# Optimization experiments

Hardware: AMD Instinct MI355X
Metric: run time of the kernel (lower is better)

## Reference

```python
import jax, jax.numpy as jnp
import numpy as np

NUM_PREFIXES = 64  # == head_dim in this config


def setup_inputs() -> dict:
    key = jax.random.key(0)
    ks = jax.random.split(key, 12)
    B, S, H = 2, 2048, 1024
    hd = NUM_PREFIXES
    nh = H // hd              # 16 heads
    din = dout = 128
    kg = H // dout            # key conv groups = 8
    P = S + hd                # position_dim = 2112
    f = jnp.float32
    sc = 0.02
    hidden = jax.random.normal(ks[0], (B, S, H), f)
    # one-hot positions: prefix tokens (first hd) use slots [S, S+hd), rest use their index
    idx = jnp.where(jnp.arange(S) < hd, S + jnp.arange(S), jnp.arange(S))
    pos = jnp.broadcast_to(jax.nn.one_hot(idx, P, dtype=f)[None], (B, S, P))
    mask = jnp.ones((B, 1, S, S), f)  # peak_into_future=True -> full visibility
    return {
        "hidden_states": hidden,
        "position_embeddings": pos,
        "attention_mask": mask,
        "Wq_head": sc * jax.random.normal(ks[1], (hd, nh, nh), f),
        "Wk_group": sc * jax.random.normal(ks[2], (kg, din, din), f),
        "Wk_head": sc * jax.random.normal(ks[3], (dout, kg, kg), f),
        "Wv_head": sc * jax.random.normal(ks[4], (hd, nh, nh), f),
        "p_attn": sc * jax.random.normal(ks[5], (3 * hd, P), f),
        "p_expand": sc * jax.random.normal(ks[6], (3, 1, nh), f),
        "Wc": sc * jax.random.normal(ks[7], (hd, nh, nh), f),
        "Wg": sc * jax.random.normal(ks[8], (2, H), f),
        "Ug": sc * jax.random.normal(ks[9], (2, H), f),
        "Vg": sc * jax.random.normal(ks[10], (2, P), f),
        "bg": jnp.zeros((2,), f),
    }


def reference(hidden_states, position_embeddings, attention_mask,
              Wq_head, Wk_group, Wk_head, Wv_head,
              p_attn, p_expand, Wc, Wg, Ug, Vg, bg):
    B, S, H = hidden_states.shape
    hd, nh, _ = Wq_head.shape
    kg, din, _ = Wk_group.shape
    npf = NUM_PREFIXES
    # LinearDescent.forward: zero out prefix-prefix attention block
    mask = attention_mask.at[:, :, :npf, :npf].set(0.0)
    # --- Attention: conv2d/per-dim head-mixing projections (proj_conv2d, proj_transpose) ---
    xh = hidden_states.reshape(B, S, nh, hd)
    q = jnp.einsum('bshd,dhg->bsgd', xh, Wq_head)      # per-dim mixing across heads
    v = jnp.einsum('bshd,dhg->bsgd', xh, Wv_head)
    # key path: per-group linear (kg groups of din), then per-dim mixing across groups
    xg = hidden_states.reshape(B, S, kg, din)
    k1 = jnp.einsum('bsgd,gde->bsge', xg, Wk_group)
    k2 = jnp.einsum('bsgd,dgh->bshd', k1, Wk_head)     # (B,S,kg,dout)
    k = k2.reshape(B, S, nh, hd)
    # positional q/k/v via p_attn (3*hd x P) + per-head expansion via p_expand (3,1,nh)
    pqkv = jnp.einsum('bsp,cp->bsc', position_embeddings, p_attn).reshape(B, S, 3, hd)
    q = q + p_expand[0, 0][None, None, :, None] * pqkv[:, :, 0][:, :, None, :]
    k = k + p_expand[1, 0][None, None, :, None] * pqkv[:, :, 1][:, :, None, :]
    v = v + p_expand[2, 0][None, None, :, None] * pqkv[:, :, 2][:, :, None, :]
    # linear (non-softmax) attention with multiplicative mask, no causal mask
    scores = jnp.einsum('bqhd,bkhd->bhqk', q, k) * mask
    ctx = jnp.einsum('bhqk,bkhd->bqhd', scores, v)
    out = jnp.einsum('bqhd,dhg->bqgd', ctx, Wc).reshape(B, S, H)
    # --- Gates: two sigmoid gates from hidden, attention output, and positions ---
    g = jax.nn.sigmoid(hidden_states @ Wg.T + out @ Ug.T + position_embeddings @ Vg.T + bg)
    return g[..., 0:1] * out + g[..., 1:2] * hidden_states
```

## Files before the change

### kernel.cpp

```cpp
#include <hip/hip_runtime.h>
#include <math.h>

#define SS   2048
#define PP   2112
#define C3   192
#define PQS  196
#define NZCAP 16

__device__ __forceinline__ void fma4s(float4& a, float s, const float4& b) {
    a.x += s*b.x; a.y += s*b.y; a.z += s*b.z; a.w += s*b.w;
}
__device__ __forceinline__ void fme4(float4& a, const float4& x, const float4& w) {
    a.x += x.x*w.x; a.y += x.y*w.y; a.z += x.z*w.z; a.w += x.w*w.w;
}
__device__ __forceinline__ float comp(const float4& v, int j) {
    return j==0 ? v.x : j==1 ? v.y : j==2 ? v.z : v.w;
}
__device__ __forceinline__ float dot4(const float4& a, const float4& b) {
    return a.x*b.x + a.y*b.y + a.z*b.z + a.w*b.w;
}

__global__ __launch_bounds__(256) void kp_prep(
    const float* __restrict__ Wq, const float* __restrict__ Wv,
    const float* __restrict__ Wc, const float* __restrict__ Wkh,
    const float* __restrict__ Wkg, const float* __restrict__ p_attn,
    const float* __restrict__ pos, const float* __restrict__ Vg,
    float* __restrict__ WqT, float* __restrict__ WvT, float* __restrict__ WcT,
    float* __restrict__ WkhT, float* __restrict__ WkgT, float* __restrict__ pqg)
{
    const int t = threadIdx.x, blk = blockIdx.x;
    if (blk < 48) {
        const float* src = (blk < 16) ? Wq : (blk < 32) ? Wv : Wc;
        float* dst = (blk < 16) ? WqT : (blk < 32) ? WvT : WcT;
        int base = (blk & 15) * 1024;
        #pragma unroll
        for (int i = 0; i < 4; ++i) {
            int didx = base + i*256 + t;
            int d = didx & 63, g = (didx>>6)&15, h = didx>>10;
            dst[didx] = src[(d<<8)+(h<<4)+g];
        }
        return;
    } else if (blk < 56) {
        int base = (blk-48)*1024;
        #pragma unroll
        for (int i = 0; i < 4; ++i) {
            int didx = base + i*256 + t;
            int dk = didx&127, hk = (didx>>7)&7, g = didx>>10;
            WkhT[didx] = Wkh[dk*64 + g*8 + hk];
        }
        return;
    } else if (blk < 184) {
        int base = (blk-56)*1024;
        #pragma unroll
        for (int i = 0; i < 4; ++i) {
            int didx = base + i*256 + t;
            int e = didx&127, g = (didx>>7)&7, d = didx>>10;
            WkgT[didx] = Wkg[(g*128+d)*128 + e];
        }
        return;
    }

    __shared__ float pq[4][C3+4];
    __shared__ int   cnt[4];
    __shared__ int   plist[4][NZCAP];
    __shared__ float vlist[4][NZCAP];
    const int row0 = (blk - 184) * 4;

    for (int i = t; i < 4*(C3+4); i += 256) ((float*)pq)[i] = 0.f;
    if (t < 4) cnt[t] = 0;
    __syncthreads();

    #pragma unroll
    for (int r = 0; r < 4; ++r) {
        const float4* prow4 = (const float4*)(pos + (size_t)(row0+r)*PP);
        #pragma unroll
        for (int c = 0; c < 3; ++c) {
            int fi = c*256 + t;
            if (fi < PP/4) {
                float4 v4 = prow4[fi];
                float vals[4] = {v4.x, v4.y, v4.z, v4.w};
                #pragma unroll
                for (int u = 0; u < 4; ++u) if (vals[u] != 0.f) {
                    int idx = atomicAdd(&cnt[r], 1);
                    if (idx < NZCAP) { plist[r][idx] = fi*4+u; vlist[r][idx] = vals[u]; }
                    else {
                        int p = fi*4+u; float val = vals[u];
                        for (int cc = 0; cc < C3; ++cc)
                            atomicAdd(&pq[r][cc], val * p_attn[(size_t)cc*PP + p]);
                        atomicAdd(&pq[r][C3],   val * Vg[p]);
                        atomicAdd(&pq[r][C3+1], val * Vg[PP+p]);
                    }
                }
            }
        }
    }
    __syncthreads();

    #pragma unroll
    for (int r = 0; r < 4; ++r) {
        int n = min(cnt[r], NZCAP);
        float acc = (t < C3+2) ? pq[r][t] : 0.f;
        for (int i = 0; i < n; ++i) {
            int p = plist[r][i]; float val = vlist[r][i];
            if (t < C3)           acc += val * p_attn[(size_t)t*PP + p];
            else if (t == C3)     acc += val * Vg[p];
            else if (t == C3+1)   acc += val * Vg[PP+p];
        }
        if (t < C3+2) pqg[(size_t)(row0+r)*PQS + t] = acc;
    }
}

__global__ __launch_bounds__(256, 4) void ka_proj(
    const float* __restrict__ hidden, const float* __restrict__ pqg,
    const float* __restrict__ WkgT, const float* __restrict__ WkhT,
    const float* __restrict__ WvT,  const float* __restrict__ p_exp,
    float* __restrict__ ko, float* __restrict__ vo)
{
    __shared__ __align__(16) float xs[4][1024];
    const int t = threadIdx.x;
    const int row0 = blockIdx.x * 4;

    #pragma unroll
    for (int i = 0; i < 4; ++i)
        ((float4*)xs)[i*256+t] = ((const float4*)hidden)[(size_t)row0*256 + i*256 + t];
    __syncthreads();

    {
        const int g = t>>4, dq = t&15;
        const float4* WvT4 = (const float4*)WvT;
        const float pev = p_exp[32+g];
        float4 av[4];
        #pragma unroll
        for (int r = 0; r < 4; ++r) {
            float4 pv = *(const float4*)(pqg + (size_t)(row0+r)*PQS + 128 + dq*4);
            av[r] = make_float4(pev*pv.x, pev*pv.y, pev*pv.z, pev*pv.w);
        }
        #pragma unroll 4
        for (int h = 0; h < 16; ++h) {
            float4 w = WvT4[(h*16+g)*16+dq];
            #pragma unroll
            for (int r = 0; r < 4; ++r)
                fme4(av[r], ((const float4*)xs[r])[h*16+dq], w);
        }
        #pragma unroll
        for (int r = 0; r < 4; ++r)
            ((float4*)vo)[(size_t)(row0+r)*256 + g*16 + dq] = av[r];
    }

    float4 a1[4] = {};
    {
        const int g8 = t>>5, eq = t&31;
        const float4* WkgT4 = (const float4*)WkgT;
        for (int dq = 0; dq < 32; ++dq) {
            float4 xq[4];
            #pragma unroll
            for (int r = 0; r < 4; ++r) xq[r] = ((const float4*)xs[r])[g8*32 + dq];
            #pragma unroll
            for (int j = 0; j < 4; ++j) {
                int d = dq*4 + j;
                float4 w = WkgT4[(d*8+g8)*32 + eq];
                #pragma unroll
                for (int r = 0; r < 4; ++r) fma4s(a1[r], comp(xq[r], j), w);
            }
        }
    }
    __syncthreads();
    {
        const int g8 = t>>5, eq = t&31;
        #pragma unroll
        for (int r = 0; r < 4; ++r)
            ((float4*)xs[r])[g8*32 + eq] = a1[r];
    }
    __syncthreads();

    {
        const int hk = t>>5, dkq = t&31;
        const int hh = hk*2 + (dkq>>4);
        const float pe = p_exp[16 + hh];
        const float4* WkhT4 = (const float4*)WkhT;
        float4 acc[4];
        #pragma unroll
        for (int r = 0; r < 4; ++r) {
            float4 pk = *(const float4*)(pqg + (size_t)(row0+r)*PQS + 64 + (dkq&15)*4);
            acc[r] = make_float4(pe*pk.x, pe*pk.y, pe*pk.z, pe*pk.w);
        }
        #pragma unroll
        for (int g = 0; g < 8; ++g) {
            float4 w = WkhT4[(g*8+hk)*32 + dkq];
            #pragma unroll
            for (int r = 0; r < 4; ++r)
                fme4(acc[r], ((const float4*)xs[r])[g*32 + dkq], w);
        }
        #pragma unroll
        for (int r = 0; r < 4; ++r)
            ((float4*)ko)[(size_t)(row0+r)*256 + hk*32 + dkq] = acc[r];
    }
}

__global__ __launch_bounds__(256) void km_kv(
    const float* __restrict__ k, const float* __restrict__ v,
    float* __restrict__ Mpart)
{
    __shared__ __align__(16) float kt[2048];
    __shared__ __align__(16) float vt[2048];
    const int t  = threadIdx.x;
    const int c  = blockIdx.x >> 5;
    const int bh = blockIdx.x & 31;
    const int b  = bh >> 4, h = bh & 15;
    const int et = t>>4, dt = t&15;
    float acc[4][4] = {};

    #pragma unroll
    for (int tile = 0; tile < 2; ++tile) {
        const int r0 = c*64 + tile*32;
        #pragma unroll
        for (int i = 0; i < 2; ++i) {
            int fi = t + 256*i;
            int r = fi>>4, q4 = fi&15;
            size_t ga = (size_t)(b*SS + r0 + r)*256 + h*16 + q4;
            ((float4*)kt)[fi] = ((const float4*)k)[ga];
            ((float4*)vt)[fi] = ((const float4*)v)[ga];
        }
        __syncthreads();
        #pragma unroll 4
        for (int r = 0; r < 32; ++r) {
            float4 kk = ((const float4*)kt)[r*16+et];
            float4 vv = ((const float4*)vt)[r*16+dt];
            float ka[4]={kk.x,kk.y,kk.z,kk.w}, va[4]={vv.x,vv.y,vv.z,vv.w};
            #pragma unroll
            for (int i2=0;i2<4;++i2)
                #pragma unroll
                for (int j=0;j<4;++j) acc[i2][j] += ka[i2]*va[j];
        }
        __syncthreads();
    }
    float4* Mc = (float4*)(Mpart + ((size_t)c*32 + bh)*4096);
    #pragma unroll
    for (int i2=0;i2<4;++i2) {
        float4 o = {acc[i2][0],acc[i2][1],acc[i2][2],acc[i2][3]};
        Mc[(et*4+i2)*16 + dt] = o;
    }
}

__global__ __launch_bounds__(256) void kr_red(
    const float* __restrict__ Mpart,
    float* __restrict__ Mfull, float* __restrict__ Mdiff)
{
    int qid = blockIdx.x*256 + threadIdx.x;
    int bh = qid >> 10, inner = qid & 1023;
    float4 s = {0,0,0,0};
    #pragma unroll
    for (int c = 1; c < 32; ++c) {
        float4 m = ((const float4*)Mpart)[(((size_t)c*32 + bh)<<10) + inner];
        s.x+=m.x; s.y+=m.y; s.z+=m.z; s.w+=m.w;
    }
    ((float4*)Mdiff)[qid] = s;
    float4 m0 = ((const float4*)Mpart)[((size_t)bh<<10) + inner];
    s.x+=m0.x; s.y+=m0.y; s.z+=m0.z; s.w+=m0.w;
    ((float4*)Mfull)[qid] = s;
}

__global__ __launch_bounds__(256, 4) void kb_out(
    const float* __restrict__ hidden, const float* __restrict__ pqg,
    const float* __restrict__ Mfull,  const float* __restrict__ Mdiff,
    const float* __restrict__ WqT,    const float* __restrict__ p_exp,
    const float* __restrict__ WcT,    const float* __restrict__ Wg,
    const float* __restrict__ Ug,     const float* __restrict__ bg,
    float* __restrict__ yo)
{
    __shared__ __align__(16) float xs[4][1024];
    __shared__ __align__(16) float qs[4][1024];
    __shared__ __align__(16) float pq0s[4][64];
    __shared__ float gs[16];
    const int t  = threadIdx.x;
    const int b  = blockIdx.x >> 9;
    const int s0 = (blockIdx.x & 511) * 4;
    const size_t rqbase = ((size_t)b*SS + s0) * 256;

    float4 xv[4];
    #pragma unroll
    for (int r = 0; r < 4; ++r) {
        xv[r] = ((const float4*)hidden)[rqbase + r*256 + t];
        ((float4*)xs[r])[t] = xv[r];
    }
    if (t < 64) {
        int r = t>>4, q = t&15;
        ((float4*)pq0s[r])[q] = *(const float4*)(pqg + (size_t)(b*SS + s0 + r)*PQS + q*4);
    }
    if (t < 16) gs[t] = 0.f;
    __syncthreads();

    const int g = t>>4, dq = t&15;

    float pW0[4], pW1[4];
    {
        float4 w0 = ((const float4*)Wg)[t], w1 = ((const float4*)Wg)[256+t];
        #pragma unroll
        for (int r = 0; r < 4; ++r) {
            pW0[r] = dot4(xv[r], w0);
            pW1[r] = dot4(xv[r], w1);
        }
    }

    {
        const float4* WqT4 = (const float4*)WqT;
        const float peq = p_exp[g];
        float4 aq[4];
        #pragma unroll
        for (int r = 0; r < 4; ++r) {
            aq[r] = make_float4(0.f, 0.f, 0.f, 0.f);
            fma4s(aq[r], peq, ((const float4*)pq0s[r])[dq]);
        }
        #pragma unroll 4
        for (int h = 0; h < 16; ++h) {
            float4 w = WqT4[(h*16+g)*16+dq];
            #pragma unroll
            for (int r = 0; r < 4; ++r)
                fme4(aq[r], ((const float4*)xs[r])[h*16+dq], w);
        }
        #pragma unroll
        for (int r = 0; r < 4; ++r) ((float4*)qs[r])[t] = aq[r];
    }
    __syncthreads();

    {
        const float* Msel = (s0 < 64) ? Mdiff : Mfull;
        const float4* Mb = (const float4*)Msel + ((size_t)b*16 + g)*1024;
        float4 acc[4] = {};
        #pragma unroll 2
        for (int eq = 0; eq < 16; ++eq) {
            float4 qq[4];
            #pragma unroll
            for (int r = 0; r < 4; ++r)
                qq[r] = ((const float4*)qs[r])[g*16 + eq];
            #pragma unroll
            for (int j = 0; j < 4; ++j) {
                float4 m = Mb[(eq*4+j)*16 + dq];
                #pragma unroll
                for (int r = 0; r < 4; ++r) fma4s(acc[r], comp(qq[r],j), m);
            }
        }
        #pragma unroll
        for (int r = 0; r < 4; ++r) ((float4*)xs[r])[t] = acc[r];
    }
    __syncthreads();

    float4 oo[4] = {};
    float pU0[4], pU1[4];
    {
        const float4* WcT4 = (const float4*)WcT;
        #pragma unroll 4
        for (int h = 0; h < 16; ++h) {
            float4 w = WcT4[(h*16+g)*16+dq];
            #pragma unroll
            for (int r = 0; r < 4; ++r)
                fme4(oo[r], ((const float4*)xs[r])[h*16+dq], w);
        }
        float4 u0 = ((const float4*)Ug)[t], u1 = ((const float4*)Ug)[256+t];
        #pragma unroll
        for (int r = 0; r < 4; ++r) {
            pU0[r] = dot4(oo[r], u0);
            pU1[r] = dot4(oo[r], u1);
        }
    }

    #pragma unroll
    for (int r = 0; r < 4; ++r) {
        float v0 = pW0[r], v1 = pW1[r], v2 = pU0[r], v3 = pU1[r];
        #pragma unroll
        for (int off = 32; off > 0; off >>= 1) {
            v0 += __shfl_down(v0, off);
            v1 += __shfl_down(v1, off);
            v2 += __shfl_down(v2, off);
            v3 += __shfl_down(v3, off);
        }
        if ((t & 63) == 0) {
            atomicAdd(&gs[r*4+0], v0);
            atomicAdd(&gs[r*4+1], v1);
            atomicAdd(&gs[r*4+2], v2);
            atomicAdd(&gs[r*4+3], v3);
        }
    }
    __syncthreads();

    #pragma unroll
    for (int r = 0; r < 4; ++r) {
        size_t grow = (size_t)b*SS + s0 + r;
        float z0 = gs[r*4+0] + gs[r*4+2] + pqg[grow*PQS + 192] + bg[0];
        float z1 = gs[r*4+1] + gs[r*4+3] + pqg[grow*PQS + 193] + bg[1];
        float G0 = 1.f/(1.f+expf(-z0));
        float G1 = 1.f/(1.f+expf(-z1));
        float4 y;
        y.x = G0*oo[r].x + G1*xv[r].x;
        y.y = G0*oo[r].y + G1*xv[r].y;
        y.z = G0*oo[r].z + G1*xv[r].z;
        y.w = G0*oo[r].w + G1*xv[r].w;
        ((float4*)yo)[rqbase + r*256 + t] = y;
    }
}

extern "C" void kernel_launch(void* const* d_in, const int* in_sizes, int n_in,
                              void* d_out, int out_size, void* d_ws, size_t ws_size,
                              hipStream_t stream)
{
    const float* hidden = (const float*)d_in[0];
    const float* pos    = (const float*)d_in[1];
    const float* Wq     = (const float*)d_in[3];
    const float* Wkg    = (const float*)d_in[4];
    const float* Wkh    = (const float*)d_in[5];
    const float* Wv     = (const float*)d_in[6];
    const float* p_attn = (const float*)d_in[7];
    const float* p_exp  = (const float*)d_in[8];
    const float* Wc     = (const float*)d_in[9];
    const float* Wg     = (const float*)d_in[10];
    const float* Ug     = (const float*)d_in[11];
    const float* Vg     = (const float*)d_in[12];
    const float* bg     = (const float*)d_in[13];

    float* ws    = (float*)d_ws;
    float* ko    = ws;
    float* vo    = ws + 4194304;
    float* Mpart = ws + 8388608;
    float* Mfull = ws + 12582912;
    float* Mdiff = ws + 12713984;
    float* pqg   = ws + 12845056;
    float* WqT   = ws + 13647872;
    float* WvT   = ws + 13664256;
    float* WcT   = ws + 13680640;
    float* WkhT  = ws + 13697024;
    float* WkgT  = ws + 13705216;

    kp_prep<<<dim3(1208), dim3(256), 0, stream>>>(Wq, Wv, Wc, Wkh, Wkg, p_attn,
                                                  pos, Vg, WqT, WvT, WcT, WkhT,
                                                  WkgT, pqg);
    ka_proj<<<dim3(1024), dim3(256), 0, stream>>>(hidden, pqg, WkgT, WkhT, WvT,
                                                  p_exp, ko, vo);
    km_kv<<<dim3(1024), dim3(256), 0, stream>>>(ko, vo, Mpart);
    kr_red<<<dim3(128), dim3(256), 0, stream>>>(Mpart, Mfull, Mdiff);
    kb_out<<<dim3(1024), dim3(256), 0, stream>>>(hidden, pqg, Mfull, Mdiff,
                                                 WqT, p_exp, WcT, Wg, Ug, bg,
                                                 (float*)d_out);
}
```

Baseline: 216.6 us.

## Fuse all five stages into one cooperative persistent kernel with grid syncs

Adds a single cooperative kernel that runs weight transposes, positional projection, K/V projection, KV outer-product partials, reduction and the output/gate stage, separated by grid-wide syncs. It keeps each block's hidden-state rows in shared memory across stages, so they are not reloaded in the final stage, and it removes four kernel launch boundaries. The old multi-kernel path remains as a fallback when cooperative launch is unavailable or fails. The cost is four grid barriers, and 1024 blocks must be co-resident (launch bounds of 4 blocks per CU), which may lower occupancy per stage.

```diff
diff --git a/kernel.cpp b/kernel.cpp
--- a/kernel.cpp
+++ b/kernel.cpp
@@ -1,5 +1,8 @@
 #include <hip/hip_runtime.h>
+#include <hip/hip_cooperative_groups.h>
 #include <math.h>
+
+namespace cg = cooperative_groups;
 
 #define SS   2048
 #define PP   2112
@@ -18,6 +21,361 @@
 }
 __device__ __forceinline__ float dot4(const float4& a, const float4& b) {
     return a.x*b.x + a.y*b.y + a.z*b.z + a.w*b.w;
+}
+
+__global__ __launch_bounds__(256, 4) void mega_ld(
+    const float* __restrict__ hidden, const float* __restrict__ pos,
+    const float* __restrict__ Wq, const float* __restrict__ Wkg,
+    const float* __restrict__ Wkh, const float* __restrict__ Wv,
+    const float* __restrict__ p_attn, const float* __restrict__ p_exp,
+    const float* __restrict__ Wc, const float* __restrict__ Wg,
+    const float* __restrict__ Ug, const float* __restrict__ Vg,
+    const float* __restrict__ bg,
+    float* __restrict__ ko, float* __restrict__ vo,
+    float* __restrict__ Mpart, float* __restrict__ Mfull,
+    float* __restrict__ Mdiff, float* __restrict__ pqg,
+    float* __restrict__ WqT, float* __restrict__ WvT,
+    float* __restrict__ WcT, float* __restrict__ WkhT,
+    float* __restrict__ WkgT, float* __restrict__ yo)
+{
+    cg::grid_group grid = cg::this_grid();
+    __shared__ __align__(16) float smem[8464];
+    float (*xs)[1024] = (float(*)[1024])smem;
+    float* region2    = smem + 4096;
+    float (*pq0s)[64] = (float(*)[64])(smem + 8192);
+    float* gs         = smem + 8448;
+
+    const int t = threadIdx.x, blk = blockIdx.x;
+    const int row0 = blk * 4;
+
+    #pragma unroll
+    for (int i = 0; i < 4; ++i)
+        ((float4*)xs)[i*256+t] = ((const float4*)hidden)[(size_t)row0*256 + i*256 + t];
+
+    if (blk < 48) {
+        const float* src = (blk < 16) ? Wq : (blk < 32) ? Wv : Wc;
+        float* dst = (blk < 16) ? WqT : (blk < 32) ? WvT : WcT;
+        int base = (blk & 15) * 1024;
+        #pragma unroll
+        for (int i = 0; i < 4; ++i) {
+            int didx = base + i*256 + t;
+            int d = didx & 63, g = (didx>>6)&15, h = didx>>10;
+            dst[didx] = src[(d<<8)+(h<<4)+g];
+        }
+    } else if (blk < 56) {
+        int base = (blk-48)*1024;
+        #pragma unroll
+        for (int i = 0; i < 4; ++i) {
+            int didx = base + i*256 + t;
+            int dk = didx&127, hk = (didx>>7)&7, g = didx>>10;
+            WkhT[didx] = Wkh[dk*64 + g*8 + hk];
+        }
+    } else if (blk < 184) {
+        int base = (blk-56)*1024;
+        #pragma unroll
+        for (int i = 0; i < 4; ++i) {
+            int didx = base + i*256 + t;
+            int e = didx&127, g = (didx>>7)&7, d = didx>>10;
+            WkgT[didx] = Wkg[(g*128+d)*128 + e];
+        }
+    }
+
+    {
+        float (*pq)[C3+4]    = (float(*)[C3+4])region2;
+        int*   cnt           = (int*)(region2 + 784);
+        int  (*plist)[NZCAP] = (int(*)[NZCAP])(region2 + 788);
+        float(*vlist)[NZCAP] = (float(*)[NZCAP])(region2 + 788 + 4*NZCAP);
+
+        for (int i = t; i < 4*(C3+4); i += 256) ((float*)pq)[i] = 0.f;
+        if (t < 4) cnt[t] = 0;
+        __syncthreads();
+
+        #pragma unroll
+        for (int r = 0; r < 4; ++r) {
+            const float4* prow4 = (const float4*)(pos + (size_t)(row0+r)*PP);
+            #pragma unroll
+            for (int c = 0; c < 3; ++c) {
+                int fi = c*256 + t;
+                if (fi < PP/4) {
+                    float4 v4 = prow4[fi];
+                    float vals[4] = {v4.x, v4.y, v4.z, v4.w};
+                    #pragma unroll
+                    for (int u = 0; u < 4; ++u) if (vals[u] != 0.f) {
+                        int idx = atomicAdd(&cnt[r], 1);
+                        if (idx < NZCAP) { plist[r][idx] = fi*4+u; vlist[r][idx] = vals[u]; }
+                        else {
+                            int p = fi*4+u; float val = vals[u];
+                            for (int cc = 0; cc < C3; ++cc)
+                                atomicAdd(&pq[r][cc], val * p_attn[(size_t)cc*PP + p]);
+                            atomicAdd(&pq[r][C3],   val * Vg[p]);
+                            atomicAdd(&pq[r][C3+1], val * Vg[PP+p]);
+                        }
+                    }
+                }
+            }
+        }
+        __syncthreads();
+
+        #pragma unroll
+        for (int r = 0; r < 4; ++r) {
+            int n = min(cnt[r], NZCAP);
+            float acc = (t < C3+2) ? pq[r][t] : 0.f;
+            for (int i = 0; i < n; ++i) {
+                int p = plist[r][i]; float val = vlist[r][i];
+                if (t < C3)           acc += val * p_attn[(size_t)t*PP + p];
+                else if (t == C3)     acc += val * Vg[p];
+                else if (t == C3+1)   acc += val * Vg[PP+p];
+            }
+            if (t < C3+2) pqg[(size_t)(row0+r)*PQS + t] = acc;
+        }
+    }
+    grid.sync();
+
+    {
+        const int g = t>>4, dq = t&15;
+        const float4* WvT4 = (const float4*)WvT;
+        const float pev = p_exp[32+g];
+        float4 av[4];
+        #pragma unroll
+        for (int r = 0; r < 4; ++r) {
+            float4 pv = *(const float4*)(pqg + (size_t)(row0+r)*PQS + 128 + dq*4);
+            av[r] = make_float4(pev*pv.x, pev*pv.y, pev*pv.z, pev*pv.w);
+        }
+        #pragma unroll 4
+        for (int h = 0; h < 16; ++h) {
+            float4 w = WvT4[(h*16+g)*16+dq];
+            #pragma unroll
+            for (int r = 0; r < 4; ++r)
+                fme4(av[r], ((const float4*)xs[r])[h*16+dq], w);
+        }
+        #pragma unroll
+        for (int r = 0; r < 4; ++r)
+            ((float4*)vo)[(size_t)(row0+r)*256 + g*16 + dq] = av[r];
+    }
+    {
+        float (*k1s)[1024] = (float(*)[1024])region2;
+        float4 a1[4] = {};
+        const int g8 = t>>5, eq = t&31;
+        const float4* WkgT4 = (const float4*)WkgT;
+        for (int dq = 0; dq < 32; ++dq) {
+            float4 xq[4];
+            #pragma unroll
+            for (int r = 0; r < 4; ++r) xq[r] = ((const float4*)xs[r])[g8*32 + dq];
+            #pragma unroll
+            for (int j = 0; j < 4; ++j) {
+                int d = dq*4 + j;
+                float4 w = WkgT4[(d*8+g8)*32 + eq];
+                #pragma unroll
+                for (int r = 0; r < 4; ++r) fma4s(a1[r], comp(xq[r], j), w);
+            }
+        }
+        #pragma unroll
+        for (int r = 0; r < 4; ++r)
+            ((float4*)k1s[r])[g8*32 + eq] = a1[r];
+        __syncthreads();
+
+        const int hk = t>>5, dkq = t&31;
+        const int hh = hk*2 + (dkq>>4);
+        const float pe = p_exp[16 + hh];
+        const float4* WkhT4 = (const float4*)WkhT;
+        float4 acc[4];
+        #pragma unroll
+        for (int r = 0; r < 4; ++r) {
+            float4 pk = *(const float4*)(pqg + (size_t)(row0+r)*PQS + 64 + (dkq&15)*4);
+            acc[r] = make_float4(pe*pk.x, pe*pk.y, pe*pk.z, pe*pk.w);
+        }
+        #pragma unroll
+        for (int g = 0; g < 8; ++g) {
+            float4 w = WkhT4[(g*8+hk)*32 + dkq];
+            #pragma unroll
+            for (int r = 0; r < 4; ++r)
+                fme4(acc[r], ((const float4*)k1s[r])[g*32 + dkq], w);
+        }
+        #pragma unroll
+        for (int r = 0; r < 4; ++r)
+            ((float4*)ko)[(size_t)(row0+r)*256 + hk*32 + dkq] = acc[r];
+    }
+    grid.sync();
+
+    {
+        float* kt = region2;
+        float* vt = region2 + 2048;
+        const int c = blk>>5, bh = blk&31, b = bh>>4, h = bh&15;
+        const int et = t>>4, dt = t&15;
+        float acc[4][4] = {};
+        #pragma unroll
+        for (int tile = 0; tile < 2; ++tile) {
+            const int r0 = c*64 + tile*32;
+            #pragma unroll
+            for (int i = 0; i < 2; ++i) {
+                int fi = t + 256*i;
+                int r = fi>>4, q4 = fi&15;
+                size_t ga = (size_t)(b*SS + r0 + r)*256 + h*16 + q4;
+                ((float4*)kt)[fi] = ((const float4*)ko)[ga];
+                ((float4*)vt)[fi] = ((const float4*)vo)[ga];
+            }
+            __syncthreads();
+            #pragma unroll 4
+            for (int r = 0; r < 32; ++r) {
+                float4 kk = ((const float4*)kt)[r*16+et];
+                float4 vv = ((const float4*)vt)[r*16+dt];
+                float ka[4]={kk.x,kk.y,kk.z,kk.w}, va[4]={vv.x,vv.y,vv.z,vv.w};
+                #pragma unroll
+                for (int i2=0;i2<4;++i2)
+                    #pragma unroll
+                    for (int j=0;j<4;++j) acc[i2][j] += ka[i2]*va[j];
+            }
+            __syncthreads();
+        }
+        float4* Mc = (float4*)(Mpart + ((size_t)c*32 + bh)*4096);
+        #pragma unroll
+        for (int i2=0;i2<4;++i2) {
+            float4 o = {acc[i2][0],acc[i2][1],acc[i2][2],acc[i2][3]};
+            Mc[(et*4+i2)*16 + dt] = o;
+        }
+    }
+    grid.sync();
+
+    if (blk < 128) {
+        int qid = blk*256 + t;
+        int bh = qid >> 10, inner = qid & 1023;
+        float4 s = {0,0,0,0};
+        #pragma unroll
+        for (int c = 1; c < 32; ++c) {
+            float4 m = ((const float4*)Mpart)[(((size_t)c*32 + bh)<<10) + inner];
+            s.x+=m.x; s.y+=m.y; s.z+=m.z; s.w+=m.w;
+        }
+        ((float4*)Mdiff)[qid] = s;
+        float4 m0 = ((const float4*)Mpart)[((size_t)bh<<10) + inner];
+        s.x+=m0.x; s.y+=m0.y; s.z+=m0.z; s.w+=m0.w;
+        ((float4*)Mfull)[qid] = s;
+    }
+    grid.sync();
+
+    {
+        float (*qs)[1024] = (float(*)[1024])region2;
+        const int b  = blk >> 9;
+        const int s0 = (blk & 511) * 4;
+        const size_t rqbase = ((size_t)b*SS + s0) * 256;
+
+        float4 xv[4];
+        #pragma unroll
+        for (int r = 0; r < 4; ++r) xv[r] = ((const float4*)xs[r])[t];
+        if (t < 64) {
+            int r = t>>4, q = t&15;
+            ((float4*)pq0s[r])[q] = *(const float4*)(pqg + (size_t)(b*SS + s0 + r)*PQS + q*4);
+        }
+        if (t < 16) gs[t] = 0.f;
+        __syncthreads();
+
+        const int g = t>>4, dq = t&15;
+
+        float pW0[4], pW1[4];
+        {
+            float4 w0 = ((const float4*)Wg)[t], w1 = ((const float4*)Wg)[256+t];
+            #pragma unroll
+            for (int r = 0; r < 4; ++r) {
+                pW0[r] = dot4(xv[r], w0);
+                pW1[r] = dot4(xv[r], w1);
+            }
+        }
+
+        {
+            const float4* WqT4 = (const float4*)WqT;
+            const float peq = p_exp[g];
+            float4 aq[4];
+            #pragma unroll
+            for (int r = 0; r < 4; ++r) {
+                aq[r] = make_float4(0.f, 0.f, 0.f, 0.f);
+                fma4s(aq[r], peq, ((const float4*)pq0s[r])[dq]);
+            }
+            #pragma unroll 4
+            for (int h = 0; h < 16; ++h) {
+                float4 w = WqT4[(h*16+g)*16+dq];
+                #pragma unroll
+                for (int r = 0; r < 4; ++r)
+                    fme4(aq[r], ((const float4*)xs[r])[h*16+dq], w);
+            }
+            #pragma unroll
+            for (int r = 0; r < 4; ++r) ((float4*)qs[r])[t] = aq[r];
+        }
+        __syncthreads();
+
+        {
+            const float* Msel = (s0 < 64) ? Mdiff : Mfull;
+            const float4* Mb = (const float4*)Msel + ((size_t)b*16 + g)*1024;
+            float4 acc[4] = {};
+            #pragma unroll 2
+            for (int eq = 0; eq < 16; ++eq) {
+                float4 qq[4];
+                #pragma unroll
+                for (int r = 0; r < 4; ++r)
+                    qq[r] = ((const float4*)qs[r])[g*16 + eq];
+                #pragma unroll
+                for (int j = 0; j < 4; ++j) {
+                    float4 m = Mb[(eq*4+j)*16 + dq];
+                    #pragma unroll
+                    for (int r = 0; r < 4; ++r) fma4s(acc[r], comp(qq[r],j), m);
+                }
+            }
+            #pragma unroll
+            for (int r = 0; r < 4; ++r) ((float4*)xs[r])[t] = acc[r];
+        }
+        __syncthreads();
+
+        float4 oo[4] = {};
+        float pU0[4], pU1[4];
+        {
+            const float4* WcT4 = (const float4*)WcT;
+            #pragma unroll 4
+            for (int h = 0; h < 16; ++h) {
+                float4 w = WcT4[(h*16+g)*16+dq];
+                #pragma unroll
+                for (int r = 0; r < 4; ++r)
+                    fme4(oo[r], ((const float4*)xs[r])[h*16+dq], w);
+            }
+            float4 u0 = ((const float4*)Ug)[t], u1 = ((const float4*)Ug)[256+t];
+            #pragma unroll
+            for (int r = 0; r < 4; ++r) {
+                pU0[r] = dot4(oo[r], u0);
+                pU1[r] = dot4(oo[r], u1);
+            }
+        }
+
+        #pragma unroll
+        for (int r = 0; r < 4; ++r) {
+            float v0 = pW0[r], v1 = pW1[r], v2 = pU0[r], v3 = pU1[r];
+            #pragma unroll
+            for (int off = 32; off > 0; off >>= 1) {
+                v0 += __shfl_down(v0, off);
+                v1 += __shfl_down(v1, off);
+                v2 += __shfl_down(v2, off);
+                v3 += __shfl_down(v3, off);
+            }
+            if ((t & 63) == 0) {
+                atomicAdd(&gs[r*4+0], v0);
+                atomicAdd(&gs[r*4+1], v1);
+                atomicAdd(&gs[r*4+2], v2);
+                atomicAdd(&gs[r*4+3], v3);
+            }
+        }
+        __syncthreads();
+
+        #pragma unroll
+        for (int r = 0; r < 4; ++r) {
+            size_t grow = (size_t)b*SS + s0 + r;
+            float z0 = gs[r*4+0] + gs[r*4+2] + pqg[grow*PQS + 192] + bg[0];
+            float z1 = gs[r*4+1] + gs[r*4+3] + pqg[grow*PQS + 193] + bg[1];
+            float G0 = 1.f/(1.f+expf(-z0));
+            float G1 = 1.f/(1.f+expf(-z1));
+            float4 y;
+            y.x = G0*oo[r].x + G1*xv[r].x;
+            y.y = G0*oo[r].y + G1*xv[r].y;
+            y.z = G0*oo[r].z + G1*xv[r].z;
+            y.w = G0*oo[r].w + G1*xv[r].w;
+            ((float4*)yo)[rqbase + r*256 + t] = y;
+        }
+    }
 }
 
 __global__ __launch_bounds__(256) void kp_prep(
@@ -429,6 +787,22 @@
     float* WcT   = ws + 13680640;
     float* WkhT  = ws + 13697024;
     float* WkgT  = ws + 13705216;
+    float* yo    = (float*)d_out;
+
+    int coop = 0;
+    hipDeviceGetAttribute(&coop, hipDeviceAttributeCooperativeLaunch, 0);
+    if (coop) {
+        void* args[] = {
+            (void*)&hidden, (void*)&pos, (void*)&Wq, (void*)&Wkg, (void*)&Wkh,
+            (void*)&Wv, (void*)&p_attn, (void*)&p_exp, (void*)&Wc, (void*)&Wg,
+            (void*)&Ug, (void*)&Vg, (void*)&bg,
+            (void*)&ko, (void*)&vo, (void*)&Mpart, (void*)&Mfull, (void*)&Mdiff,
+            (void*)&pqg, (void*)&WqT, (void*)&WvT, (void*)&WcT, (void*)&WkhT,
+            (void*)&WkgT, (void*)&yo };
+        hipError_t e = hipLaunchCooperativeKernel((void*)mega_ld, dim3(1024),
+                                                  dim3(256), args, 0, stream);
+        if (e == hipSuccess) return;
+    }
 
     kp_prep<<<dim3(1208), dim3(256), 0, stream>>>(Wq, Wv, Wc, Wkh, Wkg, p_attn,
                                                   pos, Vg, WqT, WvT, WcT, WkhT,
@@ -438,6 +812,5 @@
     km_kv<<<dim3(1024), dim3(256), 0, stream>>>(ko, vo, Mpart);
     kr_red<<<dim3(128), dim3(256), 0, stream>>>(Mpart, Mfull, Mdiff);
     kb_out<<<dim3(1024), dim3(256), 0, stream>>>(hidden, pqg, Mfull, Mdiff,
-                                                 WqT, p_exp, WcT, Wg, Ug, bg,
-                                                 (float*)d_out);
-}
+                                                 WqT, p_exp, WcT, Wg, Ug, bg, yo);
+}
```

Measured after the change: 709.3 us. 3.27x slower.
